# Kernel tuning notes

Measured on AMD Instinct MI355X. Metric: run time of the kernel, lower is better.

The kernel has to match this reference:

```python
import jax, jax.numpy as jnp
import numpy as np

N_NODES = 100_000
N_EDGES = 3_200_000
N_FEAT = 128
HIDDEN = 16
OUT = 2
N_GRAPHS = 64


def setup_inputs() -> dict:
    key = jax.random.key(0)
    ks = jax.random.split(key, 12)
    x = jax.random.normal(ks[0], (N_NODES, N_FEAT), dtype=jnp.float32)
    edge_index = jax.random.randint(ks[1], (2, N_EDGES), 0, N_NODES, dtype=jnp.int64)
    batch_idx = jnp.sort(jax.random.randint(ks[2], (N_NODES,), 0, N_GRAPHS, dtype=jnp.int64))

    def glorot(k, shape):
        s = jnp.sqrt(6.0 / (shape[0] + shape[1])).astype(jnp.float32)
        return jax.random.uniform(k, shape, jnp.float32, -1.0, 1.0) * s

    return {
        "x": x, "edge_index": edge_index, "batch_idx": batch_idx,
        "W0": glorot(ks[3], (N_FEAT, HIDDEN)), "b0": jnp.zeros((HIDDEN,), jnp.float32),
        "a0": jnp.full((1,), 0.25, jnp.float32),  # PReLU default weight
        "W1": glorot(ks[4], (HIDDEN, HIDDEN)), "b1": jnp.zeros((HIDDEN,), jnp.float32),
        "a1": jnp.full((1,), 0.25, jnp.float32),
        "W2": glorot(ks[5], (HIDDEN, HIDDEN)), "b2": jnp.zeros((HIDDEN,), jnp.float32),
        "a2": jnp.full((1,), 0.25, jnp.float32),
        "W3": glorot(ks[6], (HIDDEN, OUT)), "b3": jnp.zeros((OUT,), jnp.float32),
    }


def _prelu(x, a):
    return jnp.where(x > 0, x, a * x)


def _gcn_conv(x, W, b, src, dst, norm, n):
    # PyG GCNConv: linear transform, then normalized gather-scatter aggregation, then bias
    h = x @ W                                   # [N, out]
    msg = h[src] * norm[:, None]                # gather + per-edge scale
    out = jax.ops.segment_sum(msg, dst, num_segments=n)  # scatter-add into targets
    return out + b


def reference(x, edge_index, batch_idx, W0, b0, a0, W1, b1, a1, W2, b2, a2, W3, b3):
    n = x.shape[0]
    loop = jnp.arange(n, dtype=edge_index.dtype)
    src = jnp.concatenate([edge_index[0], loop])  # add self loops
    dst = jnp.concatenate([edge_index[1], loop])
    # symmetric degree normalization deg^-1/2 (deg over targets, all edge weights = 1)
    deg = jax.ops.segment_sum(jnp.ones_like(dst, dtype=x.dtype), dst, num_segments=n)
    dinv = jnp.where(deg > 0, jax.lax.rsqrt(deg), 0.0)
    norm = dinv[src] * dinv[dst]

    h = _prelu(_gcn_conv(x, W0, b0, src, dst, norm, n), a0)
    h = _prelu(_gcn_conv(h, W1, b1, src, dst, norm, n), a1)
    h = _prelu(_gcn_conv(h, W2, b2, src, dst, norm, n), a2)
    h = _gcn_conv(h, W3, b3, src, dst, norm, n)

    # global_mean_pool over graph ids
    sums = jax.ops.segment_sum(h, batch_idx, num_segments=N_GRAPHS)
    cnts = jax.ops.segment_sum(jnp.ones((n,), h.dtype), batch_idx, num_segments=N_GRAPHS)
    return sums / jnp.maximum(cnts, 1.0)[:, None]
```

## Files before the change

kernel.cpp:

```cpp
#include <hip/hip_runtime.h>


#define NN 100000
#define NE 3200000
#define NF 128
#define NH 16
#define NO 2
#define NG 64
#define NBLK 391
#define BN 256
#define NBUK 391
#define CHUNK 4096
#define NBLKA 782
#define CAPF 10240
#define NT0 6250

typedef __attribute__((ext_vector_type(8))) short short8;
typedef __attribute__((ext_vector_type(4))) float float4v;


__device__ __forceinline__ float ldf(const void* p, int i, int f32) {
  if (f32) return ((const float*)p)[i];
  unsigned int u = ((const unsigned short*)p)[i];
  return __uint_as_float(u << 16);
}
__device__ __forceinline__ int ldi(const void* p, int i, int i64) {
  if (i64) return (int)((const long long*)p)[i];
  return ((const int*)p)[i];
}
__device__ __forceinline__ void stf(void* p, int i, float v, int f32) {
  if (f32) {
    ((float*)p)[i] = v;
  } else {
    unsigned int w = __float_as_uint(v);
    unsigned int r = (w + 0x7fffu + ((w >> 16) & 1u)) >> 16;
    ((unsigned short*)p)[i] = (unsigned short)r;
  }
}
__device__ __forceinline__ float bf16lo(unsigned int u) { return __uint_as_float(u << 16); }
__device__ __forceinline__ float bf16hi(unsigned int u) { return __uint_as_float(u & 0xffff0000u); }
__device__ __forceinline__ unsigned int packbf(float x, float y) {
  unsigned int a = __float_as_uint(x);
  a = (a + 0x7fffu + ((a >> 16) & 1u)) >> 16;
  unsigned int b = __float_as_uint(y);
  b = (b + 0x7fffu + ((b >> 16) & 1u)) & 0xffff0000u;
  return a | b;
}
__device__ __forceinline__ int okf(float v) { return (v == v) && (fabsf(v) < 1e30f); }
__device__ __forceinline__ void nflag(int* diag, int bad, int bit) {
  if (__any(bad)) {
    if ((threadIdx.x & 63) == 0) atomicOr(diag + 2, 1 << bit);
  }
}
__device__ __forceinline__ int clampi(int v, int hi) {
  return (unsigned)v < (unsigned)hi ? v : 0;
}


__global__ __launch_bounds__(64) void k_sniff(const void* x, const void* ei, int* diag) {
  int lane = threadIdx.x;
  unsigned int xv = ((const unsigned int*)x)[lane];
  unsigned int e = (xv >> 7) & 0xffu;
  int hit = (e >= 116u && e <= 133u);
  int hits = __popcll(__ballot(hit));
  unsigned int ev = ((const unsigned int*)ei)[2 * lane + 1];
  int nzc = __popcll(__ballot(ev != 0u));
  if (lane == 0) {
    diag[0] = (hits < 32) ? 1 : 0;
    diag[1] = (nzc == 0) ? 1 : 0;
  }
}


__global__ __launch_bounds__(256) void k_build(const void* ei, const int* __restrict__ diag,
                                               int* __restrict__ cursor, int* __restrict__ ents) {
  __shared__ int ssrc[CHUNK];
  __shared__ int sdst[CHUNK];
  __shared__ int spkt[CHUNK];
  __shared__ int gpos[CHUNK];
  __shared__ int lhist[512];
  __shared__ int lcur[NBUK];
  __shared__ int goff[NBUK];
  int tid = threadIdx.x, blk = blockIdx.x;
  lhist[tid] = 0; lhist[tid + 256] = 0;
  __syncthreads();
  int i64 = diag[1];
  int base = blk * CHUNK;
  int n = NE - base; n = n > CHUNK ? CHUNK : n;
  for (int i = tid; i < n; i += 256) {
    int sv = clampi(ldi(ei, base + i, i64), NN);
    int dv = clampi(ldi(ei, NE + base + i, i64), NN);
    ssrc[i] = sv; sdst[i] = dv;
    atomicAdd(&lhist[dv >> 8], 1);
  }
  __syncthreads();
  for (int off = 1; off < 512; off <<= 1) {
    int v0 = (tid >= off) ? lhist[tid - off] : 0;
    int v1 = lhist[tid + 256 - off];
    __syncthreads();
    lhist[tid] += v0;
    lhist[tid + 256] += v1;
    __syncthreads();
  }
  for (int b = tid; b < NBUK; b += 256) {
    int incl = lhist[b];
    int excl = (b > 0) ? lhist[b - 1] : 0;
    int cnt = incl - excl;
    lcur[b] = excl;
    int rbase = cnt ? atomicAdd(&cursor[b], cnt) : 0;
    goff[b] = b * CAPF + rbase - excl;
  }
  __syncthreads();
  for (int i = tid; i < n; i += 256) {
    int dv = sdst[i], b = dv >> 8;
    int r = atomicAdd(&lcur[b], 1);
    spkt[r] = ((dv & 255) << 17) | ssrc[i];
    int gp = goff[b] + r;
    int hi = b * CAPF + CAPF - 1;
    gpos[r] = gp <= hi ? gp : hi;
  }
  __syncthreads();
  for (int i = tid; i < n; i += 256) ents[gpos[i]] = spkt[i];
}

__global__ __launch_bounds__(256) void k_bsort(int* __restrict__ ents, const int* __restrict__ cursor,
                                               int* __restrict__ rowstart, int* __restrict__ rowend,
                                               float* __restrict__ dinv, int* __restrict__ diag) {
  __shared__ int ent[CAPF];
  __shared__ int lh[BN];
  __shared__ int lcur[BN];
  int tid = threadIdx.x, b = blockIdx.x;
  int bs = b * CAPF;
  int n = cursor[b];
  if (n > CAPF) { n = CAPF; if (tid == 0) atomicOr(diag + 2, 1 << 9); }
  for (int i = tid; i < n; i += 256) ent[i] = ents[bs + i];
  lh[tid] = 0;
  __syncthreads();
  for (int i = tid; i < n; i += 256) atomicAdd(&lh[ent[i] >> 17], 1);
  __syncthreads();
  int c = lh[tid];
  for (int off = 1; off < 256; off <<= 1) {
    int v = (tid >= off) ? lh[tid - off] : 0;
    __syncthreads();
    lh[tid] += v;
    __syncthreads();
  }
  int excl = lh[tid] - c;
  lcur[tid] = excl;
  int node = (b << 8) + tid;
  if (node < NN) {
    rowstart[node] = bs + excl;
    rowend[node] = bs + excl + c;
    dinv[node] = rsqrtf((float)(c + 1));
  }
  __syncthreads();
  for (int i = tid; i < n; i += 256) {
    int e = ent[i];
    int r = atomicAdd(&lcur[e >> 17], 1);
    ents[bs + r] = e & 0x1FFFF;
  }
}


__global__ __launch_bounds__(256) void k_t0(const void* __restrict__ x, const void* __restrict__ W0,
                                            const float* __restrict__ dinv,
                                            int* __restrict__ diag, unsigned int* __restrict__ out) {
  __shared__ float ws[NF * NH];
  __shared__ float xs[16 * 129];
  int tid = threadIdx.x;
  int f32 = diag[0];
  if (!f32) {
    const unsigned short* xu = (const unsigned short*)x;
    const unsigned short* wu = (const unsigned short*)W0;
    int wave = tid >> 6, lane = tid & 63;
    int nfe = lane & 15, quad = lane >> 4;
    short8 bfr[4];
#pragma unroll
    for (int mf = 0; mf < 4; ++mf) {
      short8 t;
#pragma unroll
      for (int j = 0; j < 8; ++j) t[j] = (short)wu[(mf * 32 + quad * 8 + j) * NH + nfe];
      bfr[mf] = t;
    }
    int tile = blockIdx.x * 4 + wave;
    if (tile < NT0) {
      int node0 = tile * 16;
      const short8* xrow = (const short8*)(xu + (node0 + nfe) * NF);
      float4v c = {0.f, 0.f, 0.f, 0.f};
#pragma unroll
      for (int mf = 0; mf < 4; ++mf) {
        short8 a = xrow[mf * 4 + quad];
        c = __builtin_amdgcn_mfma_f32_16x16x32_bf16(a, bfr[mf], c, 0, 0, 0);
      }
      int bad = 0;
#pragma unroll
      for (int r = 0; r < 4; ++r) {
        int node = node0 + quad * 4 + r;
        float v = c[r] * dinv[node];
        float o = __shfl_xor(v, 1);
        if (!(nfe & 1)) out[node * 8 + (nfe >> 1)] = packbf(v, o);
        bad |= !okf(v);
      }
      nflag(diag, bad, 0);
    }
  } else {
    for (int t = 0; t < 4; ++t) {
      int tile = blockIdx.x * 4 + t;
      if (tile >= NT0) break;
      int node0 = tile * 16;
      __syncthreads();
#pragma unroll
      for (int r = 0; r < 8; ++r) ws[tid + 256 * r] = ldf(W0, tid + 256 * r, 1);
#pragma unroll
      for (int r = 0; r < 8; ++r) {
        int idx = tid + 256 * r;
        int row = idx >> 7, col = idx & 127;
        xs[row * 129 + col] = ldf(x, (node0 + row) * NF + col, 1);
      }
      __syncthreads();
      int nl = tid >> 4, f = tid & 15;
      float acc = 0.f;
#pragma unroll 4
      for (int k = 0; k < NF; ++k) acc += xs[nl * 129 + k] * ws[k * NH + f];
      acc *= dinv[node0 + nl];
      float other = __shfl_xor(acc, 1);
      if ((f & 1) == 0) out[(node0 + nl) * 8 + (f >> 1)] = packbf(acc, other);
      nflag(diag, !okf(acc), 0);
    }
  }
}


__global__ __launch_bounds__(256) void k_aggT(const unsigned int* __restrict__ hin,
                                              const int* __restrict__ srcs,
                                              const int* __restrict__ rowstart,
                                              const int* __restrict__ rowend,
                                              const float* __restrict__ dinv,
                                              const void* __restrict__ b, const void* __restrict__ a,
                                              const void* __restrict__ Wn,
                                              int* __restrict__ diag, int bit,
                                              unsigned int* __restrict__ hout) {
  __shared__ float ws[NH * NH];
  int tid = threadIdx.x;
  int f32 = diag[0];
  ws[tid] = ldf(Wn, tid, f32);
  __syncthreads();
  int gid = blockIdx.x * 256 + tid;
  int node = gid >> 3, p = gid & 7;
  unsigned int self = hin[node * 8 + p];
  float acc0 = bf16lo(self), acc1 = bf16hi(self);
  int e = rowstart[node], e1 = rowend[node];
  for (; e + 4 <= e1; e += 4) {
    int s0 = srcs[e], s1 = srcs[e + 1], s2 = srcs[e + 2], s3 = srcs[e + 3];
    unsigned int v0 = hin[s0 * 8 + p];
    unsigned int v1 = hin[s1 * 8 + p];
    unsigned int v2 = hin[s2 * 8 + p];
    unsigned int v3 = hin[s3 * 8 + p];
    acc0 += bf16lo(v0) + bf16lo(v1) + bf16lo(v2) + bf16lo(v3);
    acc1 += bf16hi(v0) + bf16hi(v1) + bf16hi(v2) + bf16hi(v3);
  }
  for (; e < e1; ++e) {
    unsigned int v = hin[srcs[e] * 8 + p];
    acc0 += bf16lo(v);
    acc1 += bf16hi(v);
  }
  float dv = dinv[node];
  float av = ldf(a, 0, f32);
  float p0 = dv * acc0 + ldf(b, 2 * p, f32);
  float p1 = dv * acc1 + ldf(b, 2 * p + 1, f32);
  p0 = p0 > 0.f ? p0 : av * p0;
  p1 = p1 > 0.f ? p1 : av * p1;
  float t0 = 0.f, t1 = 0.f;
#pragma unroll
  for (int j = 0; j < 8; ++j) {
    float qa = __shfl(p0, j, 8);
    float qb = __shfl(p1, j, 8);
    t0 += qa * ws[(2 * j) * NH + 2 * p]     + qb * ws[(2 * j + 1) * NH + 2 * p];
    t1 += qa * ws[(2 * j) * NH + 2 * p + 1] + qb * ws[(2 * j + 1) * NH + 2 * p + 1];
  }
  t0 *= dv;
  t1 *= dv;
  hout[node * 8 + p] = packbf(t0, t1);
  nflag(diag, !okf(t0) || !okf(t1), bit);
}

__global__ __launch_bounds__(256) void k_aggT3(const unsigned int* __restrict__ hin,
                                               const int* __restrict__ srcs,
                                               const int* __restrict__ rowstart,
                                               const int* __restrict__ rowend,
                                               const float* __restrict__ dinv,
                                               const void* __restrict__ b, const void* __restrict__ a,
                                               const void* __restrict__ W3,
                                               int* __restrict__ diag, float2* __restrict__ hout) {
  __shared__ float ws[NH * NO];
  int tid = threadIdx.x;
  int f32 = diag[0];
  if (tid < NH * NO) ws[tid] = ldf(W3, tid, f32);
  __syncthreads();
  int gid = blockIdx.x * 256 + tid;
  int node = gid >> 3, p = gid & 7;
  unsigned int self = hin[node * 8 + p];
  float acc0 = bf16lo(self), acc1 = bf16hi(self);
  int e = rowstart[node], e1 = rowend[node];
  for (; e + 4 <= e1; e += 4) {
    int s0 = srcs[e], s1 = srcs[e + 1], s2 = srcs[e + 2], s3 = srcs[e + 3];
    unsigned int v0 = hin[s0 * 8 + p];
    unsigned int v1 = hin[s1 * 8 + p];
    unsigned int v2 = hin[s2 * 8 + p];
    unsigned int v3 = hin[s3 * 8 + p];
    acc0 += bf16lo(v0) + bf16lo(v1) + bf16lo(v2) + bf16lo(v3);
    acc1 += bf16hi(v0) + bf16hi(v1) + bf16hi(v2) + bf16hi(v3);
  }
  for (; e < e1; ++e) {
    unsigned int v = hin[srcs[e] * 8 + p];
    acc0 += bf16lo(v);
    acc1 += bf16hi(v);
  }
  float dv = dinv[node];
  float av = ldf(a, 0, f32);
  float p0 = dv * acc0 + ldf(b, 2 * p, f32);
  float p1 = dv * acc1 + ldf(b, 2 * p + 1, f32);
  p0 = p0 > 0.f ? p0 : av * p0;
  p1 = p1 > 0.f ? p1 : av * p1;
  float u0 = p0 * ws[(2 * p) * NO] + p1 * ws[(2 * p + 1) * NO];
  float u1 = p0 * ws[(2 * p) * NO + 1] + p1 * ws[(2 * p + 1) * NO + 1];
#pragma unroll
  for (int off = 1; off < 8; off <<= 1) {
    u0 += __shfl_xor(u0, off, 8);
    u1 += __shfl_xor(u1, off, 8);
  }
  if (p == 0) hout[node] = make_float2(dv * u0, dv * u1);
  nflag(diag, !okf(u0) || !okf(u1), 6);
}

__global__ __launch_bounds__(256) void k_agg2(const float2* __restrict__ tin,
                                              const int* __restrict__ srcs,
                                              const int* __restrict__ rowstart,
                                              const int* __restrict__ rowend,
                                              const float* __restrict__ dinv,
                                              const void* __restrict__ b3,
                                              int* __restrict__ diag, float2* __restrict__ out) {
  int node = blockIdx.x * 256 + threadIdx.x;
  if (node >= NN) return;
  int f32 = diag[0];
  float2 t = tin[node];
  float a0 = t.x, a1 = t.y;
  int e = rowstart[node], e1 = rowend[node];
  for (; e + 4 <= e1; e += 4) {
    int s0 = srcs[e], s1 = srcs[e + 1], s2 = srcs[e + 2], s3 = srcs[e + 3];
    float2 h0 = tin[s0], h1 = tin[s1], h2 = tin[s2], h3 = tin[s3];
    a0 += h0.x + h1.x + h2.x + h3.x;
    a1 += h0.y + h1.y + h2.y + h3.y;
  }
  for (; e < e1; ++e) {
    float2 hv = tin[srcs[e]];
    a0 += hv.x;
    a1 += hv.y;
  }
  float dv = dinv[node];
  a0 = dv * a0 + ldf(b3, 0, f32);
  a1 = dv * a1 + ldf(b3, 1, f32);
  out[node] = make_float2(a0, a1);
  nflag(diag, !okf(a0) || !okf(a1), 7);
}


__global__ __launch_bounds__(256) void k_pool(const float2* __restrict__ h, const void* __restrict__ batch,
                                              const int* __restrict__ diag, float* __restrict__ pool) {
  __shared__ float ssum[NG * NO];
  __shared__ float scnt[NG];
  int tid = threadIdx.x;
  if (tid < NG * NO) ssum[tid] = 0.f;
  if (tid < NG) scnt[tid] = 0.f;
  __syncthreads();
  int i = blockIdx.x * 256 + tid;
  if (i < NN) {
    int i64 = diag[1];
    int g = ldi(batch, i, i64);
    g = (unsigned)g < NG ? g : 0;
    float2 v = h[i];
    atomicAdd(&ssum[g * 2], v.x);
    atomicAdd(&ssum[g * 2 + 1], v.y);
    atomicAdd(&scnt[g], 1.f);
  }
  __syncthreads();
  if (tid < NG * NO && ssum[tid] != 0.f) atomicAdd(&pool[tid], ssum[tid]);
  if (tid < NG && scnt[tid] != 0.f) atomicAdd(&pool[NG * NO + tid], scnt[tid]);
}

__global__ __launch_bounds__(128) void k_final(const float* __restrict__ pool,
                                               const int* __restrict__ diag, void* __restrict__ out) {
  int i = threadIdx.x;
  int f32 = diag[0], i64 = diag[1], stg = diag[2];
  float c = pool[NG * NO + (i >> 1)];
  c = c > 1.f ? c : 1.f;
  float v = pool[i] / c;
  if (stg != 0 || !okf(v)) {
    int stage = stg ? __ffs(stg) : 15;
    v = 1024.0f + stage * 64.0f + f32 * 16.0f + i64 * 8.0f;
  }
  stf(out, i, v, f32);
}

__global__ __launch_bounds__(128) void k_diag_ws(void* out, float v) {
  unsigned int w = __float_as_uint(v);
  ((unsigned short*)out)[threadIdx.x] = (unsigned short)(w >> 16);
}


extern "C" void kernel_launch(void* const* d_in, const int* in_sizes, int n_in,
                              void* d_out, int out_size, void* d_ws, size_t ws_size,
                              hipStream_t stream) {
  const void* x  = d_in[0];
  const void* ei = d_in[1];
  const void* batch = d_in[2];
  const void* W0 = d_in[3];
  const void* b0 = d_in[4];
  const void* a0 = d_in[5];
  const void* W1 = d_in[6];
  const void* b1 = d_in[7];
  const void* a1 = d_in[8];
  const void* W2 = d_in[9];
  const void* b2 = d_in[10];
  const void* a2 = d_in[11];
  const void* W3 = d_in[12];
  const void* b3 = d_in[13];

  char* w = (char*)d_ws;
  int* diag         = (int*)(w + 0);
  float* pool       = (float*)(w + 64);
  int* cursor       = (int*)(w + 896);
  float* dinv       = (float*)(w + 2496);
  int* rowstart     = (int*)(w + 402496);
  int* rowend       = (int*)(w + 802496);
  int* ents         = (int*)(w + 1202496);
  unsigned int* hsA = (unsigned int*)(w + 17217856);
  unsigned int* hsB = (unsigned int*)(w + 20417856);
  float2* hs3       = (float2*)(w + 23617856);
  float2* out2      = (float2*)(w + 24417856);
  const size_t NEED = 25217856;

  if (ws_size < NEED) {
    k_diag_ws<<<1, 128, 0, stream>>>(d_out, (float)ws_size);
    return;
  }

  hipMemsetAsync(d_ws, 0, 2496, stream);

  k_sniff<<<1, 64, 0, stream>>>(x, ei, diag);

  k_build<<<NBLKA, 256, 0, stream>>>(ei, diag, cursor, ents);
  k_bsort<<<NBUK, 256, 0, stream>>>(ents, cursor, rowstart, rowend, dinv, diag);

  k_t0<<<(NT0 + 3) / 4, 256, 0, stream>>>(x, W0, dinv, diag, hsA);
  k_aggT<<<NN * 8 / 256, 256, 0, stream>>>(hsA, ents, rowstart, rowend, dinv, b0, a0, W1, diag, 1, hsB);
  k_aggT<<<NN * 8 / 256, 256, 0, stream>>>(hsB, ents, rowstart, rowend, dinv, b1, a1, W2, diag, 3, hsA);
  k_aggT3<<<NN * 8 / 256, 256, 0, stream>>>(hsA, ents, rowstart, rowend, dinv, b2, a2, W3, diag, hs3);
  k_agg2<<<NBLK, 256, 0, stream>>>(hs3, ents, rowstart, rowend, dinv, b3, diag, out2);

  k_pool<<<NBLK, 256, 0, stream>>>(out2, batch, diag, pool);
  k_final<<<1, 128, 0, stream>>>(pool, diag, d_out);
}
```

Before: 318.5 us.

## Widen aggregation to 4 lanes per node, fuse final agg with pooling, rank-based CSR build

The hidden-layer aggregation kernels now use 4 lanes per node, each loading 8-byte uint2 (4 bf16 features) instead of 8 lanes with 4-byte loads. This halves the number of gather instructions and the per-edge index reads per node. The last aggregation is fused with the global mean pool, which removes one kernel launch and the round trip of the intermediate output. The build and bucket-sort kernels record each edge's rank from the counting atomic, so the second pass of shared atomics is dropped. The cost is more registers per lane and extra shared-memory arrays for the ranks.

Result: no change. 323.6 us (+1.6%).

```diff
diff --git a/kernel.cpp b/kernel.cpp
--- a/kernel.cpp
+++ b/kernel.cpp
@@ -74,15 +74,16 @@
 
 __global__ __launch_bounds__(256) void k_build(const void* ei, const int* __restrict__ diag,
                                                int* __restrict__ cursor, int* __restrict__ ents) {
-  __shared__ int ssrc[CHUNK];
-  __shared__ int sdst[CHUNK];
-  __shared__ int spkt[CHUNK];
+  __shared__ int spktA[CHUNK];
+  __shared__ unsigned short sbid[CHUNK];
+  __shared__ unsigned short srank[CHUNK];
+  __shared__ int spktB[CHUNK];
   __shared__ int gpos[CHUNK];
-  __shared__ int lhist[512];
-  __shared__ int lcur[NBUK];
+  __shared__ int lscan[512];
+  __shared__ int sexcl[NBUK];
   __shared__ int goff[NBUK];
   int tid = threadIdx.x, blk = blockIdx.x;
-  lhist[tid] = 0; lhist[tid + 256] = 0;
+  lscan[tid] = 0; lscan[tid + 256] = 0;
   __syncthreads();
   int i64 = diag[1];
   int base = blk * CHUNK;
@@ -90,63 +91,69 @@
   for (int i = tid; i < n; i += 256) {
     int sv = clampi(ldi(ei, base + i, i64), NN);
     int dv = clampi(ldi(ei, NE + base + i, i64), NN);
-    ssrc[i] = sv; sdst[i] = dv;
-    atomicAdd(&lhist[dv >> 8], 1);
+    int b = dv >> 8;
+    spktA[i] = ((dv & 255) << 17) | sv;
+    sbid[i] = (unsigned short)b;
+    srank[i] = (unsigned short)atomicAdd(&lscan[b], 1);
   }
   __syncthreads();
   for (int off = 1; off < 512; off <<= 1) {
-    int v0 = (tid >= off) ? lhist[tid - off] : 0;
-    int v1 = lhist[tid + 256 - off];
+    int v0 = (tid >= off) ? lscan[tid - off] : 0;
+    int v1 = lscan[tid + 256 - off];
     __syncthreads();
-    lhist[tid] += v0;
-    lhist[tid + 256] += v1;
+    lscan[tid] += v0;
+    lscan[tid + 256] += v1;
     __syncthreads();
   }
   for (int b = tid; b < NBUK; b += 256) {
-    int incl = lhist[b];
-    int excl = (b > 0) ? lhist[b - 1] : 0;
+    int incl = lscan[b];
+    int excl = (b > 0) ? lscan[b - 1] : 0;
     int cnt = incl - excl;
-    lcur[b] = excl;
+    sexcl[b] = excl;
     int rbase = cnt ? atomicAdd(&cursor[b], cnt) : 0;
     goff[b] = b * CAPF + rbase - excl;
   }
   __syncthreads();
   for (int i = tid; i < n; i += 256) {
-    int dv = sdst[i], b = dv >> 8;
-    int r = atomicAdd(&lcur[b], 1);
-    spkt[r] = ((dv & 255) << 17) | ssrc[i];
-    int gp = goff[b] + r;
+    int b = sbid[i];
+    int rr = sexcl[b] + srank[i];
+    spktB[rr] = spktA[i];
+    int gp = goff[b] + rr;
     int hi = b * CAPF + CAPF - 1;
-    gpos[r] = gp <= hi ? gp : hi;
-  }
-  __syncthreads();
-  for (int i = tid; i < n; i += 256) ents[gpos[i]] = spkt[i];
+    gpos[rr] = gp <= hi ? gp : hi;
+  }
+  __syncthreads();
+  for (int r = tid; r < n; r += 256) ents[gpos[r]] = spktB[r];
 }
 
 __global__ __launch_bounds__(256) void k_bsort(int* __restrict__ ents, const int* __restrict__ cursor,
                                                int* __restrict__ rowstart, int* __restrict__ rowend,
                                                float* __restrict__ dinv, int* __restrict__ diag) {
   __shared__ int ent[CAPF];
-  __shared__ int lh[BN];
-  __shared__ int lcur[BN];
+  __shared__ unsigned short rnk[CAPF];
+  __shared__ int lcnt[BN];
+  __shared__ int sexcl[BN];
   int tid = threadIdx.x, b = blockIdx.x;
   int bs = b * CAPF;
   int n = cursor[b];
   if (n > CAPF) { n = CAPF; if (tid == 0) atomicOr(diag + 2, 1 << 9); }
-  for (int i = tid; i < n; i += 256) ent[i] = ents[bs + i];
-  lh[tid] = 0;
-  __syncthreads();
-  for (int i = tid; i < n; i += 256) atomicAdd(&lh[ent[i] >> 17], 1);
-  __syncthreads();
-  int c = lh[tid];
+  lcnt[tid] = 0;
+  __syncthreads();
+  for (int i = tid; i < n; i += 256) {
+    int e = ents[bs + i];
+    ent[i] = e;
+    rnk[i] = (unsigned short)atomicAdd(&lcnt[e >> 17], 1);
+  }
+  __syncthreads();
+  int c = lcnt[tid];
   for (int off = 1; off < 256; off <<= 1) {
-    int v = (tid >= off) ? lh[tid - off] : 0;
+    int v = (tid >= off) ? lcnt[tid - off] : 0;
     __syncthreads();
-    lh[tid] += v;
+    lcnt[tid] += v;
     __syncthreads();
   }
-  int excl = lh[tid] - c;
-  lcur[tid] = excl;
+  int excl = lcnt[tid] - c;
+  sexcl[tid] = excl;
   int node = (b << 8) + tid;
   if (node < NN) {
     rowstart[node] = bs + excl;
@@ -156,8 +163,7 @@
   __syncthreads();
   for (int i = tid; i < n; i += 256) {
     int e = ent[i];
-    int r = atomicAdd(&lcur[e >> 17], 1);
-    ents[bs + r] = e & 0x1FFFF;
+    ents[bs + sexcl[e >> 17] + rnk[i]] = e & 0x1FFFF;
   }
 }
 
@@ -231,7 +237,7 @@
 }
 
 
-__global__ __launch_bounds__(256) void k_aggT(const unsigned int* __restrict__ hin,
+__global__ __launch_bounds__(256) void k_aggT(const uint2* __restrict__ hin,
                                               const int* __restrict__ srcs,
                                               const int* __restrict__ rowstart,
                                               const int* __restrict__ rowend,
@@ -239,52 +245,72 @@
                                               const void* __restrict__ b, const void* __restrict__ a,
                                               const void* __restrict__ Wn,
                                               int* __restrict__ diag, int bit,
-                                              unsigned int* __restrict__ hout) {
+                                              uint2* __restrict__ hout) {
   __shared__ float ws[NH * NH];
   int tid = threadIdx.x;
   int f32 = diag[0];
   ws[tid] = ldf(Wn, tid, f32);
   __syncthreads();
   int gid = blockIdx.x * 256 + tid;
-  int node = gid >> 3, p = gid & 7;
-  unsigned int self = hin[node * 8 + p];
-  float acc0 = bf16lo(self), acc1 = bf16hi(self);
+  if (gid >= NN * 4) return;
+  int node = gid >> 2, p = gid & 3;
+  uint2 self = hin[gid];
+  float acc0 = bf16lo(self.x), acc1 = bf16hi(self.x);
+  float acc2 = bf16lo(self.y), acc3 = bf16hi(self.y);
   int e = rowstart[node], e1 = rowend[node];
   for (; e + 4 <= e1; e += 4) {
     int s0 = srcs[e], s1 = srcs[e + 1], s2 = srcs[e + 2], s3 = srcs[e + 3];
-    unsigned int v0 = hin[s0 * 8 + p];
-    unsigned int v1 = hin[s1 * 8 + p];
-    unsigned int v2 = hin[s2 * 8 + p];
-    unsigned int v3 = hin[s3 * 8 + p];
-    acc0 += bf16lo(v0) + bf16lo(v1) + bf16lo(v2) + bf16lo(v3);
-    acc1 += bf16hi(v0) + bf16hi(v1) + bf16hi(v2) + bf16hi(v3);
+    uint2 v0 = hin[s0 * 4 + p];
+    uint2 v1 = hin[s1 * 4 + p];
+    uint2 v2 = hin[s2 * 4 + p];
+    uint2 v3 = hin[s3 * 4 + p];
+    acc0 += bf16lo(v0.x) + bf16lo(v1.x) + bf16lo(v2.x) + bf16lo(v3.x);
+    acc1 += bf16hi(v0.x) + bf16hi(v1.x) + bf16hi(v2.x) + bf16hi(v3.x);
+    acc2 += bf16lo(v0.y) + bf16lo(v1.y) + bf16lo(v2.y) + bf16lo(v3.y);
+    acc3 += bf16hi(v0.y) + bf16hi(v1.y) + bf16hi(v2.y) + bf16hi(v3.y);
   }
   for (; e < e1; ++e) {
-    unsigned int v = hin[srcs[e] * 8 + p];
-    acc0 += bf16lo(v);
-    acc1 += bf16hi(v);
+    uint2 v = hin[srcs[e] * 4 + p];
+    acc0 += bf16lo(v.x);
+    acc1 += bf16hi(v.x);
+    acc2 += bf16lo(v.y);
+    acc3 += bf16hi(v.y);
   }
   float dv = dinv[node];
   float av = ldf(a, 0, f32);
-  float p0 = dv * acc0 + ldf(b, 2 * p, f32);
-  float p1 = dv * acc1 + ldf(b, 2 * p + 1, f32);
+  float p0 = dv * acc0 + ldf(b, 4 * p + 0, f32);
+  float p1 = dv * acc1 + ldf(b, 4 * p + 1, f32);
+  float p2 = dv * acc2 + ldf(b, 4 * p + 2, f32);
+  float p3 = dv * acc3 + ldf(b, 4 * p + 3, f32);
   p0 = p0 > 0.f ? p0 : av * p0;
   p1 = p1 > 0.f ? p1 : av * p1;
-  float t0 = 0.f, t1 = 0.f;
-#pragma unroll
-  for (int j = 0; j < 8; ++j) {
-    float qa = __shfl(p0, j, 8);
-    float qb = __shfl(p1, j, 8);
-    t0 += qa * ws[(2 * j) * NH + 2 * p]     + qb * ws[(2 * j + 1) * NH + 2 * p];
-    t1 += qa * ws[(2 * j) * NH + 2 * p + 1] + qb * ws[(2 * j + 1) * NH + 2 * p + 1];
-  }
-  t0 *= dv;
-  t1 *= dv;
-  hout[node * 8 + p] = packbf(t0, t1);
-  nflag(diag, !okf(t0) || !okf(t1), bit);
-}
-
-__global__ __launch_bounds__(256) void k_aggT3(const unsigned int* __restrict__ hin,
+  p2 = p2 > 0.f ? p2 : av * p2;
+  p3 = p3 > 0.f ? p3 : av * p3;
+  float t0 = 0.f, t1 = 0.f, t2 = 0.f, t3 = 0.f;
+#pragma unroll
+  for (int j = 0; j < 4; ++j) {
+    float q0 = __shfl(p0, j, 4);
+    float q1 = __shfl(p1, j, 4);
+    float q2 = __shfl(p2, j, 4);
+    float q3 = __shfl(p3, j, 4);
+    const float* w0 = &ws[(4 * j) * NH + 4 * p];
+    const float* w1 = &ws[(4 * j + 1) * NH + 4 * p];
+    const float* w2 = &ws[(4 * j + 2) * NH + 4 * p];
+    const float* w3 = &ws[(4 * j + 3) * NH + 4 * p];
+    t0 += q0 * w0[0] + q1 * w1[0] + q2 * w2[0] + q3 * w3[0];
+    t1 += q0 * w0[1] + q1 * w1[1] + q2 * w2[1] + q3 * w3[1];
+    t2 += q0 * w0[2] + q1 * w1[2] + q2 * w2[2] + q3 * w3[2];
+    t3 += q0 * w0[3] + q1 * w1[3] + q2 * w2[3] + q3 * w3[3];
+  }
+  t0 *= dv; t1 *= dv; t2 *= dv; t3 *= dv;
+  uint2 o;
+  o.x = packbf(t0, t1);
+  o.y = packbf(t2, t3);
+  hout[gid] = o;
+  nflag(diag, !okf(t0) || !okf(t3), bit);
+}
+
+__global__ __launch_bounds__(256) void k_aggT3(const uint2* __restrict__ hin,
                                                const int* __restrict__ srcs,
                                                const int* __restrict__ rowstart,
                                                const int* __restrict__ rowend,
@@ -298,90 +324,92 @@
   if (tid < NH * NO) ws[tid] = ldf(W3, tid, f32);
   __syncthreads();
   int gid = blockIdx.x * 256 + tid;
-  int node = gid >> 3, p = gid & 7;
-  unsigned int self = hin[node * 8 + p];
-  float acc0 = bf16lo(self), acc1 = bf16hi(self);
+  if (gid >= NN * 4) return;
+  int node = gid >> 2, p = gid & 3;
+  uint2 self = hin[gid];
+  float acc0 = bf16lo(self.x), acc1 = bf16hi(self.x);
+  float acc2 = bf16lo(self.y), acc3 = bf16hi(self.y);
   int e = rowstart[node], e1 = rowend[node];
   for (; e + 4 <= e1; e += 4) {
     int s0 = srcs[e], s1 = srcs[e + 1], s2 = srcs[e + 2], s3 = srcs[e + 3];
-    unsigned int v0 = hin[s0 * 8 + p];
-    unsigned int v1 = hin[s1 * 8 + p];
-    unsigned int v2 = hin[s2 * 8 + p];
-    unsigned int v3 = hin[s3 * 8 + p];
-    acc0 += bf16lo(v0) + bf16lo(v1) + bf16lo(v2) + bf16lo(v3);
-    acc1 += bf16hi(v0) + bf16hi(v1) + bf16hi(v2) + bf16hi(v3);
+    uint2 v0 = hin[s0 * 4 + p];
+    uint2 v1 = hin[s1 * 4 + p];
+    uint2 v2 = hin[s2 * 4 + p];
+    uint2 v3 = hin[s3 * 4 + p];
+    acc0 += bf16lo(v0.x) + bf16lo(v1.x) + bf16lo(v2.x) + bf16lo(v3.x);
+    acc1 += bf16hi(v0.x) + bf16hi(v1.x) + bf16hi(v2.x) + bf16hi(v3.x);
+    acc2 += bf16lo(v0.y) + bf16lo(v1.y) + bf16lo(v2.y) + bf16lo(v3.y);
+    acc3 += bf16hi(v0.y) + bf16hi(v1.y) + bf16hi(v2.y) + bf16hi(v3.y);
   }
   for (; e < e1; ++e) {
-    unsigned int v = hin[srcs[e] * 8 + p];
-    acc0 += bf16lo(v);
-    acc1 += bf16hi(v);
+    uint2 v = hin[srcs[e] * 4 + p];
+    acc0 += bf16lo(v.x);
+    acc1 += bf16hi(v.x);
+    acc2 += bf16lo(v.y);
+    acc3 += bf16hi(v.y);
   }
   float dv = dinv[node];
   float av = ldf(a, 0, f32);
-  float p0 = dv * acc0 + ldf(b, 2 * p, f32);
-  float p1 = dv * acc1 + ldf(b, 2 * p + 1, f32);
+  float p0 = dv * acc0 + ldf(b, 4 * p + 0, f32);
+  float p1 = dv * acc1 + ldf(b, 4 * p + 1, f32);
+  float p2 = dv * acc2 + ldf(b, 4 * p + 2, f32);
+  float p3 = dv * acc3 + ldf(b, 4 * p + 3, f32);
   p0 = p0 > 0.f ? p0 : av * p0;
   p1 = p1 > 0.f ? p1 : av * p1;
-  float u0 = p0 * ws[(2 * p) * NO] + p1 * ws[(2 * p + 1) * NO];
-  float u1 = p0 * ws[(2 * p) * NO + 1] + p1 * ws[(2 * p + 1) * NO + 1];
-#pragma unroll
-  for (int off = 1; off < 8; off <<= 1) {
-    u0 += __shfl_xor(u0, off, 8);
-    u1 += __shfl_xor(u1, off, 8);
-  }
+  p2 = p2 > 0.f ? p2 : av * p2;
+  p3 = p3 > 0.f ? p3 : av * p3;
+  float u0 = p0 * ws[(4 * p) * NO]     + p1 * ws[(4 * p + 1) * NO] +
+             p2 * ws[(4 * p + 2) * NO] + p3 * ws[(4 * p + 3) * NO];
+  float u1 = p0 * ws[(4 * p) * NO + 1]     + p1 * ws[(4 * p + 1) * NO + 1] +
+             p2 * ws[(4 * p + 2) * NO + 1] + p3 * ws[(4 * p + 3) * NO + 1];
+  u0 += __shfl_xor(u0, 1, 4);
+  u0 += __shfl_xor(u0, 2, 4);
+  u1 += __shfl_xor(u1, 1, 4);
+  u1 += __shfl_xor(u1, 2, 4);
   if (p == 0) hout[node] = make_float2(dv * u0, dv * u1);
   nflag(diag, !okf(u0) || !okf(u1), 6);
 }
 
-__global__ __launch_bounds__(256) void k_agg2(const float2* __restrict__ tin,
-                                              const int* __restrict__ srcs,
-                                              const int* __restrict__ rowstart,
-                                              const int* __restrict__ rowend,
-                                              const float* __restrict__ dinv,
-                                              const void* __restrict__ b3,
-                                              int* __restrict__ diag, float2* __restrict__ out) {
-  int node = blockIdx.x * 256 + threadIdx.x;
-  if (node >= NN) return;
-  int f32 = diag[0];
-  float2 t = tin[node];
-  float a0 = t.x, a1 = t.y;
-  int e = rowstart[node], e1 = rowend[node];
-  for (; e + 4 <= e1; e += 4) {
-    int s0 = srcs[e], s1 = srcs[e + 1], s2 = srcs[e + 2], s3 = srcs[e + 3];
-    float2 h0 = tin[s0], h1 = tin[s1], h2 = tin[s2], h3 = tin[s3];
-    a0 += h0.x + h1.x + h2.x + h3.x;
-    a1 += h0.y + h1.y + h2.y + h3.y;
-  }
-  for (; e < e1; ++e) {
-    float2 hv = tin[srcs[e]];
-    a0 += hv.x;
-    a1 += hv.y;
-  }
-  float dv = dinv[node];
-  a0 = dv * a0 + ldf(b3, 0, f32);
-  a1 = dv * a1 + ldf(b3, 1, f32);
-  out[node] = make_float2(a0, a1);
-  nflag(diag, !okf(a0) || !okf(a1), 7);
-}
-
-
-__global__ __launch_bounds__(256) void k_pool(const float2* __restrict__ h, const void* __restrict__ batch,
-                                              const int* __restrict__ diag, float* __restrict__ pool) {
+__global__ __launch_bounds__(256) void k_agg2p(const float2* __restrict__ tin,
+                                               const int* __restrict__ srcs,
+                                               const int* __restrict__ rowstart,
+                                               const int* __restrict__ rowend,
+                                               const float* __restrict__ dinv,
+                                               const void* __restrict__ b3,
+                                               const void* __restrict__ batch,
+                                               int* __restrict__ diag, float* __restrict__ pool) {
   __shared__ float ssum[NG * NO];
   __shared__ float scnt[NG];
   int tid = threadIdx.x;
+  int f32 = diag[0], i64 = diag[1];
   if (tid < NG * NO) ssum[tid] = 0.f;
   if (tid < NG) scnt[tid] = 0.f;
   __syncthreads();
-  int i = blockIdx.x * 256 + tid;
-  if (i < NN) {
-    int i64 = diag[1];
-    int g = ldi(batch, i, i64);
+  int node = blockIdx.x * 256 + tid;
+  if (node < NN) {
+    float2 t = tin[node];
+    float a0 = t.x, a1 = t.y;
+    int e = rowstart[node], e1 = rowend[node];
+    for (; e + 4 <= e1; e += 4) {
+      int s0 = srcs[e], s1 = srcs[e + 1], s2 = srcs[e + 2], s3 = srcs[e + 3];
+      float2 h0 = tin[s0], h1 = tin[s1], h2 = tin[s2], h3 = tin[s3];
+      a0 += h0.x + h1.x + h2.x + h3.x;
+      a1 += h0.y + h1.y + h2.y + h3.y;
+    }
+    for (; e < e1; ++e) {
+      float2 hv = tin[srcs[e]];
+      a0 += hv.x;
+      a1 += hv.y;
+    }
+    float dv = dinv[node];
+    a0 = dv * a0 + ldf(b3, 0, f32);
+    a1 = dv * a1 + ldf(b3, 1, f32);
+    int g = ldi(batch, node, i64);
     g = (unsigned)g < NG ? g : 0;
-    float2 v = h[i];
-    atomicAdd(&ssum[g * 2], v.x);
-    atomicAdd(&ssum[g * 2 + 1], v.y);
+    atomicAdd(&ssum[g * 2], a0);
+    atomicAdd(&ssum[g * 2 + 1], a1);
     atomicAdd(&scnt[g], 1.f);
+    nflag(diag, !okf(a0) || !okf(a1), 7);
   }
   __syncthreads();
   if (tid < NG * NO && ssum[tid] != 0.f) atomicAdd(&pool[tid], ssum[tid]);
@@ -434,11 +462,10 @@
   int* rowstart     = (int*)(w + 402496);
   int* rowend       = (int*)(w + 802496);
   int* ents         = (int*)(w + 1202496);
-  unsigned int* hsA = (unsigned int*)(w + 17217856);
-  unsigned int* hsB = (unsigned int*)(w + 20417856);
+  uint2* hsA        = (uint2*)(w + 17217856);
+  uint2* hsB        = (uint2*)(w + 20417856);
   float2* hs3       = (float2*)(w + 23617856);
-  float2* out2      = (float2*)(w + 24417856);
-  const size_t NEED = 25217856;
+  const size_t NEED = 24417856;
 
   if (ws_size < NEED) {
     k_diag_ws<<<1, 128, 0, stream>>>(d_out, (float)ws_size);
@@ -452,12 +479,11 @@
   k_build<<<NBLKA, 256, 0, stream>>>(ei, diag, cursor, ents);
   k_bsort<<<NBUK, 256, 0, stream>>>(ents, cursor, rowstart, rowend, dinv, diag);
 
-  k_t0<<<(NT0 + 3) / 4, 256, 0, stream>>>(x, W0, dinv, diag, hsA);
-  k_aggT<<<NN * 8 / 256, 256, 0, stream>>>(hsA, ents, rowstart, rowend, dinv, b0, a0, W1, diag, 1, hsB);
-  k_aggT<<<NN * 8 / 256, 256, 0, stream>>>(hsB, ents, rowstart, rowend, dinv, b1, a1, W2, diag, 3, hsA);
-  k_aggT3<<<NN * 8 / 256, 256, 0, stream>>>(hsA, ents, rowstart, rowend, dinv, b2, a2, W3, diag, hs3);
-  k_agg2<<<NBLK, 256, 0, stream>>>(hs3, ents, rowstart, rowend, dinv, b3, diag, out2);
-
-  k_pool<<<NBLK, 256, 0, stream>>>(out2, batch, diag, pool);
+  k_t0<<<(NT0 + 3) / 4, 256, 0, stream>>>(x, W0, dinv, diag, (unsigned int*)hsA);
+  k_aggT<<<(NN * 4 + 255) / 256, 256, 0, stream>>>(hsA, ents, rowstart, rowend, dinv, b0, a0, W1, diag, 1, hsB);
+  k_aggT<<<(NN * 4 + 255) / 256, 256, 0, stream>>>(hsB, ents, rowstart, rowend, dinv, b1, a1, W2, diag, 3, hsA);
+  k_aggT3<<<(NN * 4 + 255) / 256, 256, 0, stream>>>(hsA, ents, rowstart, rowend, dinv, b2, a2, W3, diag, hs3);
+  k_agg2p<<<NBLK, 256, 0, stream>>>(hs3, ents, rowstart, rowend, dinv, b3, batch, diag, pool);
+
   k_final<<<1, 128, 0, stream>>>(pool, diag, d_out);
 }
```
